# Optimization experiments

Measured on AMD Instinct MI355X. Metric: run time of the kernel, lower is better.

## Reference

```python
import jax, jax.numpy as jnp
import numpy as np

B, S, D = 2, 2048, 1024
H, DH = 16, 64
E, K, FH = 8, 2, 4096
AUX_W = 0.01
EPS = 1e-6


def setup_inputs() -> dict:
    key = jax.random.key(0)
    ks = jax.random.split(key, 20)
    init = lambda k, shape: (jax.random.normal(k, shape, dtype=jnp.float32) * 0.02)
    return {
        'x': jax.random.normal(ks[0], (B, S, D), dtype=jnp.float32),
        'ln1_s': jnp.ones((D,), jnp.float32), 'ln1_b': jnp.zeros((D,), jnp.float32),
        'Wq': init(ks[1], (D, H * DH)), 'bq': jnp.zeros((H * DH,), jnp.float32),
        'Wk': init(ks[2], (D, H * DH)), 'bk': jnp.zeros((H * DH,), jnp.float32),
        'Wv': init(ks[3], (D, H * DH)), 'bv': jnp.zeros((H * DH,), jnp.float32),
        'Wo': init(ks[4], (H * DH, D)), 'bo': jnp.zeros((D,), jnp.float32),
        'ln2_s': jnp.ones((D,), jnp.float32), 'ln2_b': jnp.zeros((D,), jnp.float32),
        'Wg': init(ks[5], (D, E)), 'bg': jnp.zeros((E,), jnp.float32),
        'W1': init(ks[6], (E, D, FH)), 'b1': jnp.zeros((E, FH), jnp.float32),
        'W2': init(ks[7], (E, FH, D)), 'b2': jnp.zeros((E, D), jnp.float32),
    }


def _layer_norm(x, scale, bias):
    mu = jnp.mean(x, axis=-1, keepdims=True)
    var = jnp.mean(jnp.square(x - mu), axis=-1, keepdims=True)
    return (x - mu) * jax.lax.rsqrt(var + EPS) * scale + bias


def _causal_attn(x, Wq, bq, Wk, bk, Wv, bv, Wo, bo):
    b, s, _ = x.shape
    q = (x @ Wq + bq).reshape(b, s, H, DH)
    k = (x @ Wk + bk).reshape(b, s, H, DH)
    v = (x @ Wv + bv).reshape(b, s, H, DH)
    scores = jnp.einsum('bqhd,bkhd->bhqk', q, k) / jnp.sqrt(jnp.float32(DH))
    causal = jnp.tril(jnp.ones((s, s), dtype=bool))
    scores = jnp.where(causal, scores, jnp.finfo(scores.dtype).min)
    attn = jax.nn.softmax(scores, axis=-1)
    out = jnp.einsum('bhqk,bkhd->bqhd', attn, v).reshape(b, s, H * DH)
    return out @ Wo + bo


def _moe(x, Wg, bg, W1, b1, W2, b2):
    # x: (B,S,D) -> tokens (T,D)
    T = x.shape[0] * x.shape[1]
    xf = x.reshape(T, D)
    logits = xf @ Wg + bg                      # (T,E)
    probs = jax.nn.softmax(logits, axis=-1)
    topv, topi = jax.lax.top_k(probs, K)       # (T,K)
    topv = topv / jnp.sum(topv, axis=-1, keepdims=True)
    combine = jnp.zeros((T, E), xf.dtype).at[jnp.arange(T)[:, None], topi].set(topv)
    out = jnp.zeros((T, D), xf.dtype)
    for e in range(E):  # fixed small expert loop
        h = jax.nn.gelu(xf @ W1[e] + b1[e])
        out = out + combine[:, e:e + 1] * (h @ W2[e] + b2[e])
    # load-balance aux loss
    frac = jnp.mean((combine > 0).astype(jnp.float32), axis=0)
    pmean = jnp.mean(probs, axis=0)
    aux = AUX_W * E * jnp.sum(frac * pmean)
    return out.reshape(x.shape), aux


def reference(x, ln1_s, ln1_b, Wq, bq, Wk, bk, Wv, bv, Wo, bo,
              ln2_s, ln2_b, Wg, bg, W1, b1, W2, b2):
    working = x
    attn_in = _layer_norm(working, ln1_s, ln1_b)
    attn_out = _causal_attn(attn_in, Wq, bq, Wk, bk, Wv, bv, Wo, bo)
    working = working + attn_out
    ffn_in = _layer_norm(working, ln2_s, ln2_b)
    ffn_out, aux = _moe(ffn_in, Wg, bg, W1, b1, W2, b2)
    output = working + ffn_out
    return output, aux
```

## Files before the change

### kernel.cpp

```cpp
#include <hip/hip_runtime.h>
#include <hip/hip_bf16.h>
#include <math.h>

#define Bb 2
#define Ss 2048
#define Dd 1024
#define Hh 16
#define DH 64
#define Ee 8
#define FH 4096
#define Tt (Bb*Ss)

typedef __attribute__((ext_vector_type(8))) short short8;
typedef __attribute__((ext_vector_type(4))) short short4v;
typedef __attribute__((ext_vector_type(4))) float float4v;

static __device__ inline short f2bf(float f) {
    __hip_bfloat16 h = __float2bfloat16(f);
    return *reinterpret_cast<short*>(&h);
}

static __device__ inline void glds16(const __hip_bfloat16* g, __hip_bfloat16* l) {
    __builtin_amdgcn_global_load_lds(
        (const __attribute__((address_space(1))) unsigned int*)g,
        (__attribute__((address_space(3))) unsigned int*)l, 16, 0, 0);
}

__global__ __launch_bounds__(256) void ln_kernel(const float* __restrict__ x,
                                                 const float* __restrict__ sc,
                                                 const float* __restrict__ bi,
                                                 __hip_bfloat16* __restrict__ y) {
    int t = blockIdx.x, tid = threadIdx.x;
    const float* xr = x + (size_t)t * Dd;
    float s1 = 0.f, s2 = 0.f;
    for (int d = tid; d < Dd; d += 256) { float v = xr[d]; s1 += v; s2 += v * v; }
    __shared__ float r1[256], r2[256];
    r1[tid] = s1; r2[tid] = s2; __syncthreads();
    for (int off = 128; off > 0; off >>= 1) {
        if (tid < off) { r1[tid] += r1[tid + off]; r2[tid] += r2[tid + off]; }
        __syncthreads();
    }
    float mu = r1[0] * (1.f / Dd);
    float var = r2[0] * (1.f / Dd) - mu * mu;
    float rstd = rsqrtf(var + 1e-6f);
    __hip_bfloat16* yr = y + (size_t)t * Dd;
    for (int d = tid; d < Dd; d += 256) {
        float v = xr[d];
        yr[d] = __float2bfloat16((v - mu) * rstd * sc[d] + bi[d]);
    }
}

__global__ __launch_bounds__(256) void transpose_qkvo(
    const float* W0, const float* W1, const float* W2, const float* W3,
    __hip_bfloat16* T0, __hip_bfloat16* T1, __hip_bfloat16* T2, __hip_bfloat16* T3) {
    int z = blockIdx.z;
    const float* W = (z == 0) ? W0 : (z == 1) ? W1 : (z == 2) ? W2 : W3;
    __hip_bfloat16* Wt = (z == 0) ? T0 : (z == 1) ? T1 : (z == 2) ? T2 : T3;
    __shared__ float tile[32][33];
    int k0 = blockIdx.y * 32, n0 = blockIdx.x * 32;
    int tx = threadIdx.x & 31, ty = threadIdx.x >> 5;
    #pragma unroll
    for (int p = 0; p < 4; p++)
        tile[ty + p * 8][tx] = W[(size_t)(k0 + ty + p * 8) * Dd + n0 + tx];
    __syncthreads();
    #pragma unroll
    for (int p = 0; p < 4; p++)
        Wt[(size_t)(n0 + ty + p * 8) * Dd + k0 + tx] = __float2bfloat16(tile[tx][ty + p * 8]);
}

__global__ __launch_bounds__(256) void transpose_we(const float* __restrict__ W,
                                                    __hip_bfloat16* __restrict__ Wt,
                                                    int Kd, int N) {
    int e = blockIdx.z;
    W  += (size_t)e * Kd * N;
    Wt += (size_t)e * Kd * N;
    __shared__ float tile[32][33];
    int k0 = blockIdx.y * 32, n0 = blockIdx.x * 32;
    int tx = threadIdx.x & 31, ty = threadIdx.x >> 5;
    #pragma unroll
    for (int p = 0; p < 4; p++)
        tile[ty + p * 8][tx] = W[(size_t)(k0 + ty + p * 8) * N + n0 + tx];
    __syncthreads();
    #pragma unroll
    for (int p = 0; p < 4; p++)
        Wt[(size_t)(n0 + ty + p * 8) * Kd + k0 + tx] = __float2bfloat16(tile[tx][ty + p * 8]);
}

template<int MODE>
__global__ __launch_bounds__(256) void gemm_mfma(
    const __hip_bfloat16* __restrict__ A, const __hip_bfloat16* __restrict__ Bt,
    const float* __restrict__ bias, void* __restrict__ Cv,
    int M, int N, int Kd,
    const int* __restrict__ bucket, const int* __restrict__ cnts,
    const int* __restrict__ bases, const float* __restrict__ residual)
{
    int Me = M;
    const int* rowIdx = nullptr;
    int hbase = 0;
    if (MODE == 2 || MODE == 3) {
        int e = blockIdx.z;
        Me = cnts[e];
        hbase = bases[e];
        Bt += (size_t)e * N * Kd;
        bias += (size_t)e * N;
        if (MODE == 2) rowIdx = bucket + e * Tt;
        if (MODE == 3) A += (size_t)hbase * Kd;
    }
    int m0 = blockIdx.y * 128;
    if (m0 >= Me) return;
    int n0 = blockIdx.x * 128;

    __shared__ __hip_bfloat16 As[2 * 128 * 32];
    __shared__ __hip_bfloat16 Bs[2 * 128 * 32];

    int tid = threadIdx.x;
    int lane = tid & 63, wave = tid >> 6;
    int wm = (wave & 1) * 64, wn = (wave >> 1) * 64;
    int quad = lane >> 4, l16 = lane & 15;

    int rs = lane >> 2;
    int sslot = (lane & 3) ^ ((lane >> 3) & 3);
    int rowS0 = 16 * (2 * wave + 0) + rs;
    int rowS1 = 16 * (2 * wave + 1) + rs;

    const __hip_bfloat16 *gA0, *gA1;
    if (MODE == 2) {
        int g0 = m0 + rowS0, g1 = m0 + rowS1;
        int r0 = (g0 < Me) ? rowIdx[g0] : 0;
        int r1 = (g1 < Me) ? rowIdx[g1] : 0;
        gA0 = A + (size_t)r0 * Kd + sslot * 8;
        gA1 = A + (size_t)r1 * Kd + sslot * 8;
    } else {
        gA0 = A + (size_t)(m0 + rowS0) * Kd + sslot * 8;
        gA1 = A + (size_t)(m0 + rowS1) * Kd + sslot * 8;
    }
    const __hip_bfloat16* gB0 = Bt + (size_t)(n0 + rowS0) * Kd + sslot * 8;
    const __hip_bfloat16* gB1 = Bt + (size_t)(n0 + rowS1) * Kd + sslot * 8;

    __hip_bfloat16* lA0 = As + (2 * wave + 0) * 512;
    __hip_bfloat16* lA1 = As + (2 * wave + 1) * 512;
    __hip_bfloat16* lB0 = Bs + (2 * wave + 0) * 512;
    __hip_bfloat16* lB1 = Bs + (2 * wave + 1) * 512;

    int rsw = (l16 >> 1) & 3;
    int rdoff = (quad ^ rsw) * 8;

    float4v acc[4][4];
    #pragma unroll
    for (int i = 0; i < 4; i++)
        #pragma unroll
        for (int j = 0; j < 4; j++) acc[i][j] = (float4v)0.f;

    glds16(gA0, lA0);
    glds16(gA1, lA1);
    glds16(gB0, lB0);
    glds16(gB1, lB1);
    __syncthreads();

    const int NT = Kd >> 5;
    int cur = 0;
    for (int t = 0; t < NT; t++) {
        if (t + 1 < NT) {
            int ko = (t + 1) << 5;
            int bo = (cur ^ 1) * 4096;
            glds16(gA0 + ko, lA0 + bo);
            glds16(gA1 + ko, lA1 + bo);
            glds16(gB0 + ko, lB0 + bo);
            glds16(gB1 + ko, lB1 + bo);
        }
        int cb = cur * 4096;
        short8 af[4], bf[4];
        #pragma unroll
        for (int i = 0; i < 4; i++)
            af[i] = *(const short8*)(&As[cb + (wm + i * 16 + l16) * 32 + rdoff]);
        #pragma unroll
        for (int j = 0; j < 4; j++)
            bf[j] = *(const short8*)(&Bs[cb + (wn + j * 16 + l16) * 32 + rdoff]);
        #pragma unroll
        for (int i = 0; i < 4; i++)
            #pragma unroll
            for (int j = 0; j < 4; j++)
                acc[i][j] = __builtin_amdgcn_mfma_f32_16x16x32_bf16(af[i], bf[j], acc[i][j], 0, 0, 0);
        __syncthreads();
        cur ^= 1;
    }

    #pragma unroll
    for (int i = 0; i < 4; i++) {
        #pragma unroll
        for (int j = 0; j < 4; j++) {
            int col = n0 + wn + j * 16 + l16;
            float bsv = bias[col];
            if (MODE == 4) {
                int mb = m0 + wm + i * 16 + quad * 4;
                int b = mb >> 11, s0 = mb & (Ss - 1);
                int h = col >> 6, d = col & (DH - 1);
                short4v pk;
                #pragma unroll
                for (int r = 0; r < 4; r++) pk[r] = f2bf(acc[i][j][r] + bsv);
                *(short4v*)((__hip_bfloat16*)Cv + ((size_t)(b * Hh + h) * DH + d) * Ss + s0) = pk;
                continue;
            }
            #pragma unroll
            for (int r = 0; r < 4; r++) {
                int m = m0 + wm + i * 16 + quad * 4 + r;
                if (m >= Me) continue;
                float val = acc[i][j][r] + bsv;
                if (MODE == 0) {
                    ((__hip_bfloat16*)Cv)[(size_t)m * N + col] = __float2bfloat16(val);
                } else if (MODE == 1) {
                    ((float*)Cv)[(size_t)m * N + col] = val + residual[(size_t)m * N + col];
                } else if (MODE == 2) {
                    float z = 0.7978845608028654f * (val + 0.044715f * val * val * val);
                    float eg = __expf(2.f * z);
                    float th = 1.f - __fdividef(2.f, eg + 1.f);
                    ((__hip_bfloat16*)Cv)[(size_t)(hbase + m) * N + col] =
                        __float2bfloat16(0.5f * val * (1.f + th));
                } else {
                    ((float*)Cv)[(size_t)(hbase + m) * N + col] = val;
                }
            }
        }
    }
}

__global__ __launch_bounds__(256) void attn_mfma(const __hip_bfloat16* __restrict__ q,
                                                 const __hip_bfloat16* __restrict__ k,
                                                 const __hip_bfloat16* __restrict__ Vt,
                                                 __hip_bfloat16* __restrict__ out) {
    int h = blockIdx.x, tile = blockIdx.y, b = blockIdx.z;
    int wave = threadIdx.x >> 6, lane = threadIdx.x & 63;
    int quad = lane >> 4, l16 = lane & 15;
    int q0 = tile * 64 + wave * 16;
    int tb = b * Ss;

    __shared__ __hip_bfloat16 Ks[32 * 72];
    __shared__ __hip_bfloat16 Vs[64 * 40];

    const __hip_bfloat16* qp = q + (size_t)(tb + q0 + l16) * (Hh * DH) + h * DH + quad * 8;
    short8 qf0 = *(const short8*)(qp);
    short8 qf1 = *(const short8*)(qp + 32);

    float4v oc[4];
    #pragma unroll
    for (int i = 0; i < 4; i++) oc[i] = (float4v)0.f;
    float lsum = 0.f;

    const __hip_bfloat16* kbase = k + (size_t)tb * (Hh * DH) + h * DH;
    const __hip_bfloat16* vbase = Vt + ((size_t)(b * Hh + h) * DH) * Ss;
    int qglob = q0 + l16;
    int srcA = (quad & 1) * 32 + l16;
    int srcB = srcA + 16;
    int sel = quad >> 1;
    int nsteps = 2 * tile + 2;

    int krow = threadIdx.x >> 3, kg = threadIdx.x & 7;
    int vd   = threadIdx.x >> 2, vg = threadIdx.x & 3;

    short8 kv = *(const short8*)(kbase + (size_t)krow * (Hh * DH) + kg * 8);
    short8 vv = *(const short8*)(vbase + (size_t)vd * Ss + vg * 8);

    for (int st = 0; st < nsteps; st++) {
        int k0 = st * 32;
        *(short8*)(&Ks[krow * 72 + kg * 8]) = kv;
        *(short8*)(&Vs[vd * 40 + vg * 8]) = vv;
        __syncthreads();
        if (st + 1 < nsteps) {
            kv = *(const short8*)(kbase + (size_t)(k0 + 32 + krow) * (Hh * DH) + kg * 8);
            vv = *(const short8*)(vbase + (size_t)vd * Ss + (k0 + 32) + vg * 8);
        }

        short8 a0 = *(const short8*)(&Ks[l16 * 72 + quad * 8]);
        short8 a1 = *(const short8*)(&Ks[l16 * 72 + 32 + quad * 8]);
        short8 a2 = *(const short8*)(&Ks[(l16 + 16) * 72 + quad * 8]);
        short8 a3 = *(const short8*)(&Ks[(l16 + 16) * 72 + 32 + quad * 8]);

        float4v c0 = (float4v)0.f, c1 = (float4v)0.f;
        c0 = __builtin_amdgcn_mfma_f32_16x16x32_bf16(a0, qf0, c0, 0, 0, 0);
        c0 = __builtin_amdgcn_mfma_f32_16x16x32_bf16(a1, qf1, c0, 0, 0, 0);
        c1 = __builtin_amdgcn_mfma_f32_16x16x32_bf16(a2, qf0, c1, 0, 0, 0);
        c1 = __builtin_amdgcn_mfma_f32_16x16x32_bf16(a3, qf1, c1, 0, 0, 0);

        float p0[4], p1[4];
        #pragma unroll
        for (int r = 0; r < 4; r++) {
            int key0 = k0 + quad * 4 + r;
            int key1 = key0 + 16;
            p0[r] = (key0 <= qglob) ? __expf(c0[r] * 0.125f - 4.f) : 0.f;
            p1[r] = (key1 <= qglob) ? __expf(c1[r] * 0.125f - 4.f) : 0.f;
            lsum += p0[r] + p1[r];
        }

        short8 pf;
        #pragma unroll
        for (int r = 0; r < 4; r++) {
            float t0 = __shfl(p0[r], srcA), t1 = __shfl(p1[r], srcA);
            pf[r] = f2bf(sel ? t1 : t0);
            float u0 = __shfl(p0[r], srcB), u1 = __shfl(p1[r], srcB);
            pf[4 + r] = f2bf(sel ? u1 : u0);
        }

        #pragma unroll
        for (int nt = 0; nt < 4; nt++) {
            short8 bv = *(const short8*)(&Vs[(nt * 16 + l16) * 40 + quad * 8]);
            oc[nt] = __builtin_amdgcn_mfma_f32_16x16x32_bf16(pf, bv, oc[nt], 0, 0, 0);
        }
        __syncthreads();
    }

    lsum += __shfl_xor(lsum, 16);
    lsum += __shfl_xor(lsum, 32);
    float linv[4];
    #pragma unroll
    for (int r = 0; r < 4; r++) linv[r] = 1.f / __shfl(lsum, quad * 4 + r);

    #pragma unroll
    for (int nt = 0; nt < 4; nt++) {
        #pragma unroll
        for (int r = 0; r < 4; r++) {
            int tokq = tb + q0 + quad * 4 + r;
            out[(size_t)tokq * (Hh * DH) + h * DH + nt * 16 + l16] =
                __float2bfloat16(oc[nt][r] * linv[r]);
        }
    }
}

#define GT 64
__global__ __launch_bounds__(256) void gate_kernel(const float* __restrict__ wk,
                                                   const float* __restrict__ g2s,
                                                   const float* __restrict__ g2b,
                                                   const float* __restrict__ Wg,
                                                   const float* __restrict__ bg,
                                                   float* __restrict__ psum,
                                                   int* __restrict__ counts,
                                                   int* __restrict__ bucket,
                                                   int* __restrict__ eidx,
                                                   int* __restrict__ epos,
                                                   float* __restrict__ ew) {
    int t0 = blockIdx.x * GT;
    int wave = threadIdx.x >> 6, lane = threadIdx.x & 63;

    __shared__ float sp[GT][Ee];
    __shared__ int   sel_e[2][GT];
    __shared__ int   spos[2][GT];
    __shared__ int   lbase[Ee];

    for (int i = wave; i < GT; i += 4) {
        int t = t0 + i;
        const float* xr = wk + (size_t)t * Dd;
        float xv[16];
        float s1 = 0.f, sq = 0.f;
        #pragma unroll
        for (int j = 0; j < 16; j++) {
            float v = xr[lane + j * 64];
            xv[j] = v; s1 += v; sq += v * v;
        }
        #pragma unroll
        for (int off = 32; off; off >>= 1) { s1 += __shfl_xor(s1, off); sq += __shfl_xor(sq, off); }
        float mu = s1 * (1.f / Dd), var = sq * (1.f / Dd) - mu * mu;
        float rstd = rsqrtf(var + 1e-6f);
        float acc[Ee] = {};
        #pragma unroll
        for (int j = 0; j < 16; j++) {
            int d = lane + j * 64;
            float xn = (xv[j] - mu) * rstd * g2s[d] + g2b[d];
            const float* wr = Wg + d * Ee;
            #pragma unroll
            for (int e = 0; e < Ee; e++) acc[e] += xn * wr[e];
        }
        #pragma unroll
        for (int e = 0; e < Ee; e++)
            #pragma unroll
            for (int off = 32; off; off >>= 1) acc[e] += __shfl_xor(acc[e], off);
        if (lane == 0) {
            float lg[Ee], mx = -1e30f;
            #pragma unroll
            for (int e = 0; e < Ee; e++) { lg[e] = acc[e] + bg[e]; mx = fmaxf(mx, lg[e]); }
            float p[Ee], ssum = 0.f;
            #pragma unroll
            for (int e = 0; e < Ee; e++) { p[e] = __expf(lg[e] - mx); ssum += p[e]; }
            float ise = 1.f / ssum;
            #pragma unroll
            for (int e = 0; e < Ee; e++) { p[e] *= ise; sp[i][e] = p[e]; }
            int e1 = 0;
            for (int e = 1; e < Ee; e++) if (p[e] > p[e1]) e1 = e;
            int e2 = -1;
            for (int e = 0; e < Ee; e++) if (e != e1 && (e2 < 0 || p[e] > p[e2])) e2 = e;
            sel_e[0][i] = e1; sel_e[1][i] = e2;
            float w1 = p[e1], w2 = p[e2], isw = 1.f / (w1 + w2);
            eidx[2 * t] = e1; ew[2 * t] = w1 * isw;
            eidx[2 * t + 1] = e2; ew[2 * t + 1] = w2 * isw;
        }
    }
    __syncthreads();

    if (threadIdx.x < Ee) {
        int e = threadIdx.x;
        int local = 0;
        for (int i = 0; i < GT; i++) {
            if (sel_e[0][i] == e) spos[0][i] = local++;
            if (sel_e[1][i] == e) spos[1][i] = local++;
        }
        lbase[e] = atomicAdd(&counts[e], local);
        float ps = 0.f;
        for (int i = 0; i < GT; i++) ps += sp[i][e];
        atomicAdd(&psum[e], ps);
    }
    __syncthreads();

    if (threadIdx.x < GT) {
        int i = threadIdx.x, t = t0 + i;
        #pragma unroll
        for (int s = 0; s < 2; s++) {
            int e = sel_e[s][i];
            int pos = lbase[e] + spos[s][i];
            bucket[e * Tt + pos] = t;
            epos[2 * t + s] = pos;
        }
    }
}

__global__ void zero_init(float* psum, int* counts) {
    int i = threadIdx.x;
    if (i < Ee) { psum[i] = 0.f; counts[i] = 0; }
}

__global__ void prefix_kernel(const int* counts, int* bases) {
    if (threadIdx.x == 0) {
        int run = 0;
        for (int e = 0; e < Ee; e++) { bases[e] = run; run += counts[e]; }
    }
}

__global__ __launch_bounds__(256) void combine_out(const float* __restrict__ working,
                                                   const float* __restrict__ O2,
                                                   const int* __restrict__ bases,
                                                   const int* __restrict__ eidx,
                                                   const int* __restrict__ epos,
                                                   const float* __restrict__ ew,
                                                   float* __restrict__ out) {
    int t = blockIdx.x, tid = threadIdx.x;
    int e0 = eidx[2 * t], e1 = eidx[2 * t + 1];
    size_t r0 = (size_t)(bases[e0] + epos[2 * t]) * Dd;
    size_t r1 = (size_t)(bases[e1] + epos[2 * t + 1]) * Dd;
    float w0 = ew[2 * t], w1 = ew[2 * t + 1];
    const float4* wr = (const float4*)(working + (size_t)t * Dd);
    const float4* o0 = (const float4*)(O2 + r0);
    const float4* o1 = (const float4*)(O2 + r1);
    float4* dst = (float4*)(out + (size_t)t * Dd);
    float4 a = wr[tid], x0 = o0[tid], x1 = o1[tid];
    dst[tid] = make_float4(a.x + w0 * x0.x + w1 * x1.x,
                           a.y + w0 * x0.y + w1 * x1.y,
                           a.z + w0 * x0.z + w1 * x1.z,
                           a.w + w0 * x0.w + w1 * x1.w);
}

__global__ void aux_kernel(const int* counts, const float* psum, float* out) {
    if (threadIdx.x == 0 && blockIdx.x == 0) {
        float a = 0.f;
        for (int e = 0; e < Ee; e++)
            a += (counts[e] * (1.f / Tt)) * (psum[e] * (1.f / Tt));
        out[0] = 0.01f * (float)Ee * a;
    }
}

extern "C" void kernel_launch(void* const* d_in, const int* in_sizes, int n_in,
                              void* d_out, int out_size, void* d_ws, size_t ws_size,
                              hipStream_t stream) {
    const float* x     = (const float*)d_in[0];
    const float* ln1_s = (const float*)d_in[1];
    const float* ln1_b = (const float*)d_in[2];
    const float* Wq    = (const float*)d_in[3];
    const float* bq    = (const float*)d_in[4];
    const float* Wk    = (const float*)d_in[5];
    const float* bk    = (const float*)d_in[6];
    const float* Wv    = (const float*)d_in[7];
    const float* bv    = (const float*)d_in[8];
    const float* Wo    = (const float*)d_in[9];
    const float* bo    = (const float*)d_in[10];
    const float* ln2_s = (const float*)d_in[11];
    const float* ln2_b = (const float*)d_in[12];
    const float* Wg    = (const float*)d_in[13];
    const float* bg    = (const float*)d_in[14];
    const float* W1    = (const float*)d_in[15];
    const float* b1    = (const float*)d_in[16];
    const float* W2    = (const float*)d_in[17];
    const float* b2    = (const float*)d_in[18];

    const size_t MBy = 1u << 20;
    char* base = (char*)d_ws;
    __hip_bfloat16* attn_in = (__hip_bfloat16*)(base);
    __hip_bfloat16* qbf     = (__hip_bfloat16*)(base + 8 * MBy);
    __hip_bfloat16* kbf     = (__hip_bfloat16*)(base + 16 * MBy);
    __hip_bfloat16* Vt      = (__hip_bfloat16*)(base + 24 * MBy);
    float*          working = (float*)(base + 32 * MBy);
    __hip_bfloat16* ffn_in  = (__hip_bfloat16*)(base + 48 * MBy);
    __hip_bfloat16* Hbuf    = (__hip_bfloat16*)(base + 56 * MBy);
    float*          O2      = (float*)(base);
    __hip_bfloat16* WT      = (__hip_bfloat16*)(base + 120 * MBy);
    __hip_bfloat16* WqT     = (__hip_bfloat16*)(base + 120 * MBy);
    __hip_bfloat16* WkT     = (__hip_bfloat16*)(base + 122 * MBy);
    __hip_bfloat16* WvT     = (__hip_bfloat16*)(base + 124 * MBy);
    __hip_bfloat16* WoT     = (__hip_bfloat16*)(base + 126 * MBy);
    char* rt = base + 184 * MBy;
    int*   bucket = (int*)rt;
    int*   counts = (int*)(rt + Ee * Tt * 4);
    int*   bases  = counts + 64;
    float* psum   = (float*)(bases + 64);
    int*   eidx   = (int*)(psum + 64);
    int*   epos   = eidx + 2 * Tt;
    float* ew     = (float*)(epos + 2 * Tt);

    float* out  = (float*)d_out;
    float* auxp = out + (size_t)Tt * Dd;

    zero_init<<<1, 64, 0, stream>>>(psum, counts);
    transpose_qkvo<<<dim3(32, 32, 4), 256, 0, stream>>>(Wq, Wk, Wv, Wo, WqT, WkT, WvT, WoT);
    ln_kernel<<<Tt, 256, 0, stream>>>(x, ln1_s, ln1_b, attn_in);

    dim3 gqkv(Dd / 128, Tt / 128);
    gemm_mfma<0><<<gqkv, 256, 0, stream>>>(attn_in, WqT, bq, qbf, Tt, Dd, Dd,
                                           nullptr, nullptr, nullptr, nullptr);
    gemm_mfma<0><<<gqkv, 256, 0, stream>>>(attn_in, WkT, bk, kbf, Tt, Dd, Dd,
                                           nullptr, nullptr, nullptr, nullptr);
    gemm_mfma<4><<<gqkv, 256, 0, stream>>>(attn_in, WvT, bv, Vt, Tt, Dd, Dd,
                                           nullptr, nullptr, nullptr, nullptr);

    attn_mfma<<<dim3(Hh, Ss / 64, Bb), 256, 0, stream>>>(qbf, kbf, Vt, attn_in);

    gemm_mfma<1><<<gqkv, 256, 0, stream>>>(attn_in, WoT, bo, working, Tt, Dd, Dd,
                                           nullptr, nullptr, nullptr, x);

    ln_kernel<<<Tt, 256, 0, stream>>>(working, ln2_s, ln2_b, ffn_in);
    gate_kernel<<<Tt / GT, 256, 0, stream>>>(working, ln2_s, ln2_b, Wg, bg,
                                             psum, counts, bucket, eidx, epos, ew);
    prefix_kernel<<<1, 64, 0, stream>>>(counts, bases);

    transpose_we<<<dim3(FH / 32, Dd / 32, Ee), 256, 0, stream>>>(W1, WT, Dd, FH);
    gemm_mfma<2><<<dim3(FH / 128, Tt / 128, Ee), 256, 0, stream>>>(
        ffn_in, WT, b1, Hbuf, Tt, FH, Dd, bucket, counts, bases, nullptr);
    transpose_we<<<dim3(Dd / 32, FH / 32, Ee), 256, 0, stream>>>(W2, WT, FH, Dd);
    gemm_mfma<3><<<dim3(Dd / 128, Tt / 128, Ee), 256, 0, stream>>>(
        Hbuf, WT, b2, O2, Tt, Dd, FH, bucket, counts, bases, nullptr);

    combine_out<<<Tt, 256, 0, stream>>>(working, O2, bases, eidx, epos, ew, out);
    aux_kernel<<<1, 64, 0, stream>>>(counts, psum, auxp);
}
```

Measured before the change: 887.3 us.

## Fuse QKV projections into one launch and split-K the second expert GEMM

Merges the three Q/K/V projection GEMMs into a single launch that uses blockIdx.z to select the weight, bias and output layout. This relies on WqT, WkT and WvT sitting contiguously in the workspace. When the workspace is large enough, the expert down-projection GEMM (K=4096) is split into two K halves written to separate buffers, and combine_out sums them. The split doubles the block count to improve occupancy on imbalanced expert loads, at the cost of extra fp32 partial writes and reads.

```diff
diff --git a/kernel.cpp b/kernel.cpp
--- a/kernel.cpp
+++ b/kernel.cpp
@@ -86,25 +86,36 @@
         Wt[(size_t)(n0 + ty + p * 8) * Kd + k0 + tx] = __float2bfloat16(tile[tx][ty + p * 8]);
 }
 
-template<int MODE>
+template<int MODE, int NS = 1>
 __global__ __launch_bounds__(256) void gemm_mfma(
     const __hip_bfloat16* __restrict__ A, const __hip_bfloat16* __restrict__ Bt,
     const float* __restrict__ bias, void* __restrict__ Cv,
     int M, int N, int Kd,
     const int* __restrict__ bucket, const int* __restrict__ cnts,
-    const int* __restrict__ bases, const float* __restrict__ residual)
+    const int* __restrict__ bases, const float* __restrict__ residual,
+    const float* __restrict__ bias_k, const float* __restrict__ bias_v,
+    void* __restrict__ Ck, void* __restrict__ Cv2)
 {
     int Me = M;
     const int* rowIdx = nullptr;
     int hbase = 0;
+    int ksplit = 0;
+    int zsel = 0;
     if (MODE == 2 || MODE == 3) {
-        int e = blockIdx.z;
+        int e = (NS == 2) ? (blockIdx.z >> 1) : blockIdx.z;
+        if (NS == 2) ksplit = blockIdx.z & 1;
         Me = cnts[e];
         hbase = bases[e];
         Bt += (size_t)e * N * Kd;
         bias += (size_t)e * N;
         if (MODE == 2) rowIdx = bucket + e * Tt;
         if (MODE == 3) A += (size_t)hbase * Kd;
+    }
+    if (MODE == 5) {
+        zsel = blockIdx.z;
+        Bt += (size_t)zsel * Dd * Dd;
+        if (zsel == 1) bias = bias_k;
+        if (zsel == 2) bias = bias_v;
     }
     int m0 = blockIdx.y * 128;
     if (m0 >= Me) return;
@@ -151,16 +162,22 @@
         #pragma unroll
         for (int j = 0; j < 4; j++) acc[i][j] = (float4v)0.f;
 
-    glds16(gA0, lA0);
-    glds16(gA1, lA1);
-    glds16(gB0, lB0);
-    glds16(gB1, lB1);
+    const int NT = Kd >> 5;
+    int t0s = 0, t1s = NT;
+    if (NS == 2) { int hlf = NT >> 1; t0s = ksplit * hlf; t1s = t0s + hlf; }
+
+    {
+        int ko = t0s << 5;
+        glds16(gA0 + ko, lA0);
+        glds16(gA1 + ko, lA1);
+        glds16(gB0 + ko, lB0);
+        glds16(gB1 + ko, lB1);
+    }
     __syncthreads();
 
-    const int NT = Kd >> 5;
     int cur = 0;
-    for (int t = 0; t < NT; t++) {
-        if (t + 1 < NT) {
+    for (int t = t0s; t < t1s; t++) {
+        if (t + 1 < t1s) {
             int ko = (t + 1) << 5;
             int bo = (cur ^ 1) * 4096;
             glds16(gA0 + ko, lA0 + bo);
@@ -190,15 +207,16 @@
         #pragma unroll
         for (int j = 0; j < 4; j++) {
             int col = n0 + wn + j * 16 + l16;
-            float bsv = bias[col];
-            if (MODE == 4) {
+            float bsv = (MODE == 3 && NS == 2 && ksplit == 1) ? 0.f : bias[col];
+            if (MODE == 4 || (MODE == 5 && zsel == 2)) {
+                __hip_bfloat16* vt = (__hip_bfloat16*)((MODE == 5) ? Cv2 : Cv);
                 int mb = m0 + wm + i * 16 + quad * 4;
                 int b = mb >> 11, s0 = mb & (Ss - 1);
                 int h = col >> 6, d = col & (DH - 1);
                 short4v pk;
                 #pragma unroll
                 for (int r = 0; r < 4; r++) pk[r] = f2bf(acc[i][j][r] + bsv);
-                *(short4v*)((__hip_bfloat16*)Cv + ((size_t)(b * Hh + h) * DH + d) * Ss + s0) = pk;
+                *(short4v*)(vt + ((size_t)(b * Hh + h) * DH + d) * Ss + s0) = pk;
                 continue;
             }
             #pragma unroll
@@ -208,6 +226,9 @@
                 float val = acc[i][j][r] + bsv;
                 if (MODE == 0) {
                     ((__hip_bfloat16*)Cv)[(size_t)m * N + col] = __float2bfloat16(val);
+                } else if (MODE == 5) {
+                    __hip_bfloat16* co = (__hip_bfloat16*)((zsel == 0) ? Cv : Ck);
+                    co[(size_t)m * N + col] = __float2bfloat16(val);
                 } else if (MODE == 1) {
                     ((float*)Cv)[(size_t)m * N + col] = val + residual[(size_t)m * N + col];
                 } else if (MODE == 2) {
@@ -217,7 +238,8 @@
                     ((__hip_bfloat16*)Cv)[(size_t)(hbase + m) * N + col] =
                         __float2bfloat16(0.5f * val * (1.f + th));
                 } else {
-                    ((float*)Cv)[(size_t)(hbase + m) * N + col] = val;
+                    float* o3 = (float*)((NS == 2 && ksplit == 1) ? Cv2 : Cv);
+                    o3[(size_t)(hbase + m) * N + col] = val;
                 }
             }
         }
@@ -434,11 +456,13 @@
 
 __global__ __launch_bounds__(256) void combine_out(const float* __restrict__ working,
                                                    const float* __restrict__ O2,
+                                                   const float* __restrict__ O2b,
                                                    const int* __restrict__ bases,
                                                    const int* __restrict__ eidx,
                                                    const int* __restrict__ epos,
                                                    const float* __restrict__ ew,
-                                                   float* __restrict__ out) {
+                                                   float* __restrict__ out,
+                                                   int ns) {
     int t = blockIdx.x, tid = threadIdx.x;
     int e0 = eidx[2 * t], e1 = eidx[2 * t + 1];
     size_t r0 = (size_t)(bases[e0] + epos[2 * t]) * Dd;
@@ -447,8 +471,15 @@
     const float4* wr = (const float4*)(working + (size_t)t * Dd);
     const float4* o0 = (const float4*)(O2 + r0);
     const float4* o1 = (const float4*)(O2 + r1);
+    float4 a = wr[tid], x0 = o0[tid], x1 = o1[tid];
+    if (ns == 2) {
+        const float4* p0 = (const float4*)(O2b + r0);
+        const float4* p1 = (const float4*)(O2b + r1);
+        float4 y0 = p0[tid], y1 = p1[tid];
+        x0.x += y0.x; x0.y += y0.y; x0.z += y0.z; x0.w += y0.w;
+        x1.x += y1.x; x1.y += y1.y; x1.z += y1.z; x1.w += y1.w;
+    }
     float4* dst = (float4*)(out + (size_t)t * Dd);
-    float4 a = wr[tid], x0 = o0[tid], x1 = o1[tid];
     dst[tid] = make_float4(a.x + w0 * x0.x + w1 * x1.x,
                            a.y + w0 * x0.y + w1 * x1.y,
                            a.z + w0 * x0.z + w1 * x1.z,
@@ -511,6 +542,9 @@
     int*   epos   = eidx + 2 * Tt;
     float* ew     = (float*)(epos + 2 * Tt);
 
+    bool   sk  = (ws_size >= (size_t)224 * MBy);
+    float* O2b = sk ? (float*)(base + 192 * MBy) : O2;
+
     float* out  = (float*)d_out;
     float* auxp = out + (size_t)Tt * Dd;
 
@@ -519,17 +553,15 @@
     ln_kernel<<<Tt, 256, 0, stream>>>(x, ln1_s, ln1_b, attn_in);
 
     dim3 gqkv(Dd / 128, Tt / 128);
-    gemm_mfma<0><<<gqkv, 256, 0, stream>>>(attn_in, WqT, bq, qbf, Tt, Dd, Dd,
+    gemm_mfma<5><<<dim3(Dd / 128, Tt / 128, 3), 256, 0, stream>>>(
+        attn_in, WqT, bq, qbf, Tt, Dd, Dd,
+        nullptr, nullptr, nullptr, nullptr, bk, bv, kbf, Vt);
+
+    attn_mfma<<<dim3(Hh, Ss / 64, Bb), 256, 0, stream>>>(qbf, kbf, Vt, attn_in);
+
+    gemm_mfma<1><<<gqkv, 256, 0, stream>>>(attn_in, WoT, bo, working, Tt, Dd, Dd,
+                                           nullptr, nullptr, nullptr, x,
                                            nullptr, nullptr, nullptr, nullptr);
-    gemm_mfma<0><<<gqkv, 256, 0, stream>>>(attn_in, WkT, bk, kbf, Tt, Dd, Dd,
-                                           nullptr, nullptr, nullptr, nullptr);
-    gemm_mfma<4><<<gqkv, 256, 0, stream>>>(attn_in, WvT, bv, Vt, Tt, Dd, Dd,
-                                           nullptr, nullptr, nullptr, nullptr);
-
-    attn_mfma<<<dim3(Hh, Ss / 64, Bb), 256, 0, stream>>>(qbf, kbf, Vt, attn_in);
-
-    gemm_mfma<1><<<gqkv, 256, 0, stream>>>(attn_in, WoT, bo, working, Tt, Dd, Dd,
-                                           nullptr, nullptr, nullptr, x);
 
     ln_kernel<<<Tt, 256, 0, stream>>>(working, ln2_s, ln2_b, ffn_in);
     gate_kernel<<<Tt / GT, 256, 0, stream>>>(working, ln2_s, ln2_b, Wg, bg,
@@ -538,11 +570,20 @@
 
     transpose_we<<<dim3(FH / 32, Dd / 32, Ee), 256, 0, stream>>>(W1, WT, Dd, FH);
     gemm_mfma<2><<<dim3(FH / 128, Tt / 128, Ee), 256, 0, stream>>>(
-        ffn_in, WT, b1, Hbuf, Tt, FH, Dd, bucket, counts, bases, nullptr);
+        ffn_in, WT, b1, Hbuf, Tt, FH, Dd, bucket, counts, bases, nullptr,
+        nullptr, nullptr, nullptr, nullptr);
     transpose_we<<<dim3(Dd / 32, FH / 32, Ee), 256, 0, stream>>>(W2, WT, FH, Dd);
-    gemm_mfma<3><<<dim3(Dd / 128, Tt / 128, Ee), 256, 0, stream>>>(
-        Hbuf, WT, b2, O2, Tt, Dd, FH, bucket, counts, bases, nullptr);
-
-    combine_out<<<Tt, 256, 0, stream>>>(working, O2, bases, eidx, epos, ew, out);
+    if (sk) {
+        gemm_mfma<3, 2><<<dim3(Dd / 128, Tt / 128, 2 * Ee), 256, 0, stream>>>(
+            Hbuf, WT, b2, O2, Tt, Dd, FH, bucket, counts, bases, nullptr,
+            nullptr, nullptr, nullptr, O2b);
+    } else {
+        gemm_mfma<3, 1><<<dim3(Dd / 128, Tt / 128, Ee), 256, 0, stream>>>(
+            Hbuf, WT, b2, O2, Tt, Dd, FH, bucket, counts, bases, nullptr,
+            nullptr, nullptr, nullptr, nullptr);
+    }
+
+    combine_out<<<Tt, 256, 0, stream>>>(working, O2, O2b, bases, eidx, epos, ew, out,
+                                        sk ? 2 : 1);
     aux_kernel<<<1, 64, 0, stream>>>(counts, psum, auxp);
 }
```

Result: faster. 848.9 us (-4.3%).
